# Kernel optimization log

Measured on AMD Instinct MI355X. Metric: run time of the kernel, lower is better.

Reference implementation:

```python
import jax, jax.numpy as jnp
import numpy as np

N_BINS = 64
SIGMA_SCALE = 0.5
EPS = 1e-8


def _radial_weights(H, W, dtype=jnp.float32):
    r_max = min(H, W) / 2.0 - 1.0
    yy, xx = jnp.meshgrid(jnp.arange(H, dtype=dtype), jnp.arange(W, dtype=dtype), indexing='ij')
    cx, cy = (W - 1) / 2.0, (H - 1) / 2.0
    r = jnp.sqrt((xx - cx) ** 2 + (yy - cy) ** 2)  # (H, W)
    edges = jnp.linspace(0.0, r_max, N_BINS + 1, dtype=dtype)
    centers = 0.5 * (edges[:-1] + edges[1:])  # (B,)
    bin_width = r_max / N_BINS
    sigma = SIGMA_SCALE * bin_width + EPS
    Wmat = jnp.exp(-0.5 * ((r[:, :, None] - centers) / sigma) ** 2)  # (H, W, B)
    return Wmat, centers


def setup_inputs() -> dict:
    key = jax.random.key(0)
    k1, k2 = jax.random.split(key)
    shape = (32, 12, 256, 256)
    pred = jax.random.uniform(k1, shape, dtype=jnp.float32)
    target = jax.random.uniform(k2, shape, dtype=jnp.float32)
    return {"pred": pred, "target": target}


def reference(pred, target):
    N, WVL, H, W = pred.shape
    Wmat, centers = _radial_weights(H, W, pred.dtype)
    Wflat = Wmat.reshape(H * W, N_BINS)            # (HW, B)
    den = jnp.maximum(Wflat.sum(axis=0), EPS)      # (B,)
    # broadcast-multiply-reduce expressed as a GEMM: (N*WVL, HW) @ (HW, B)
    Xf = pred.reshape(N, WVL, H * W)
    Yf = target.reshape(N, WVL, H * W)
    prof_pred = jnp.einsum('nwp,pb->nwb', Xf, Wflat) / den
    prof_targ = jnp.einsum('nwp,pb->nwb', Yf, Wflat) / den
    # bin_weight == 'r': weight by bin-center radius, normalized to unit mean
    w = centers[None, None, :]
    w = w / jnp.maximum(w.mean(axis=-1, keepdims=True), EPS)  # (1,1,B)
    # loss == 'fvu'
    y = prof_targ
    ybar = y.mean(axis=-1, keepdims=True)
    sse = (w * (prof_pred - y) ** 2).sum(axis=-1)
    ssy = jnp.maximum((w * (y - ybar) ** 2).sum(axis=-1), EPS)
    return (sse / ssy).mean()
```

## Files before the change

### kernel.cpp

```cpp
#include <hip/hip_runtime.h>
#include <math.h>


#define NBINS 64
#define WIN   8
#define G     4
#define NIMG  384
#define HDIM  256
#define WDIM  256
#define BANDS 8
#define BANDROWS 32

#define DEN_BANDS 128
#define DEN_ROWS  2

#define LOG2E 1.4426950408889634f
#define EXP_M4 0.018315638888734179f

__device__ __forceinline__ float fexp2(float x) {
#if __has_builtin(__builtin_amdgcn_exp2f)
  return __builtin_amdgcn_exp2f(x);
#else
  return exp2f(x);
#endif
}

__global__ __launch_bounds__(256) void radial_prof_kernel(
    const float* __restrict__ pred,
    const float* __restrict__ targ,
    float* __restrict__ prof)
{
  const int x     = threadIdx.x;
  const int band  = blockIdx.x & (BANDS - 1);
  const int chunk = blockIdx.x >> 3;
  const int g0    = chunk * G;

  __shared__ float hist[G][2][NBINS];
  for (int i = threadIdx.x; i < G * 2 * NBINS; i += 256) ((float*)hist)[i] = 0.f;
  __syncthreads();

  const float dx     = (float)x - 127.5f;
  const float dx2    = dx * dx;
  const int   y0     = band * BANDROWS;
  const float inv_bw = 64.0f / 127.0f;

  float acc[G][2][WIN];
  #pragma unroll
  for (int g = 0; g < G; ++g)
    #pragma unroll
    for (int i = 0; i < 2; ++i)
      #pragma unroll
      for (int s = 0; s < WIN; ++s) acc[g][i][s] = 0.f;

  int k0;
  {
    const float dy = (float)y0 - 127.5f;
    k0 = (int)floorf(sqrtf(dx2 + dy * dy) * inv_bw) - 3;
  }

  const size_t istr = (size_t)HDIM * WDIM;
  const float* pp = pred + (size_t)g0 * istr + (size_t)y0 * WDIM + x;
  const float* tp = targ + (size_t)g0 * istr + (size_t)y0 * WDIM + x;

  for (int yi = 0; yi < BANDROWS; ++yi) {
    const float dy = (float)(y0 + yi) - 127.5f;
    const float r  = sqrtf(dx2 + dy * dy);
    const float u  = r * inv_bw;
    const float fl = floorf(u);
    const int   k  = (int)fl - 3;

    if (k != k0) {
      if (k == k0 + 1) {
        if ((unsigned)k0 < NBINS) {
          #pragma unroll
          for (int g = 0; g < G; ++g) {
            atomicAdd(&hist[g][0][k0], acc[g][0][0]);
            atomicAdd(&hist[g][1][k0], acc[g][1][0]);
          }
        }
        #pragma unroll
        for (int g = 0; g < G; ++g)
          #pragma unroll
          for (int i = 0; i < 2; ++i) {
            #pragma unroll
            for (int s = 0; s < WIN - 1; ++s) acc[g][i][s] = acc[g][i][s + 1];
            acc[g][i][WIN - 1] = 0.f;
          }
      } else if (k == k0 - 1) {
        const int bh = k0 + WIN - 1;
        if ((unsigned)bh < NBINS) {
          #pragma unroll
          for (int g = 0; g < G; ++g) {
            atomicAdd(&hist[g][0][bh], acc[g][0][WIN - 1]);
            atomicAdd(&hist[g][1][bh], acc[g][1][WIN - 1]);
          }
        }
        #pragma unroll
        for (int g = 0; g < G; ++g)
          #pragma unroll
          for (int i = 0; i < 2; ++i) {
            #pragma unroll
            for (int s = WIN - 1; s > 0; --s) acc[g][i][s] = acc[g][i][s - 1];
            acc[g][i][0] = 0.f;
          }
      } else {
        #pragma unroll
        for (int s = 0; s < WIN; ++s) {
          const int b = k0 + s;
          if ((unsigned)b < NBINS) {
            #pragma unroll
            for (int g = 0; g < G; ++g) {
              atomicAdd(&hist[g][0][b], acc[g][0][s]);
              atomicAdd(&hist[g][1][b], acc[g][1][s]);
            }
          }
        }
        #pragma unroll
        for (int g = 0; g < G; ++g)
          #pragma unroll
          for (int i = 0; i < 2; ++i)
            #pragma unroll
            for (int s = 0; s < WIN; ++s) acc[g][i][s] = 0.f;
      }
      k0 = k;
    }

    if (k0 < NBINS) {
      const float t0 = (u - fl) + 2.5f;
      float w = fexp2(-(2.0f * LOG2E) * t0 * t0);
      float m = fexp2((4.0f * t0 - 2.0f) * LOG2E);
      float xp[G], xt[G];
      #pragma unroll
      for (int g = 0; g < G; ++g) {
        xp[g] = pp[(size_t)g * istr];
        xt[g] = tp[(size_t)g * istr];
      }
      #pragma unroll
      for (int s = 0; s < WIN; ++s) {
        #pragma unroll
        for (int g = 0; g < G; ++g) {
          acc[g][0][s] = fmaf(w, xp[g], acc[g][0][s]);
          acc[g][1][s] = fmaf(w, xt[g], acc[g][1][s]);
        }
        w *= m;
        m *= EXP_M4;
      }
    }
    pp += WDIM; tp += WDIM;
  }

  #pragma unroll
  for (int s = 0; s < WIN; ++s) {
    const int b = k0 + s;
    if ((unsigned)b < NBINS) {
      #pragma unroll
      for (int g = 0; g < G; ++g) {
        atomicAdd(&hist[g][0][b], acc[g][0][s]);
        atomicAdd(&hist[g][1][b], acc[g][1][s]);
      }
    }
  }
  __syncthreads();

  for (int i = threadIdx.x; i < G * 2 * NBINS; i += 256)
    atomicAdd(&prof[(size_t)g0 * 2 * NBINS + i], ((float*)hist)[i]);
}

__global__ __launch_bounds__(256) void den_kernel(float* __restrict__ den)
{
  const int x    = threadIdx.x;
  const int band = blockIdx.x;
  __shared__ float hist[NBINS];
  if (threadIdx.x < NBINS) hist[threadIdx.x] = 0.f;
  __syncthreads();

  const float dx     = (float)x - 127.5f;
  const float dx2    = dx * dx;
  const int   y0     = band * DEN_ROWS;
  const float inv_bw = 64.0f / 127.0f;

  float acc[WIN];
  #pragma unroll
  for (int s = 0; s < WIN; ++s) acc[s] = 0.f;

  int k0;
  {
    const float dy = (float)y0 - 127.5f;
    k0 = (int)floorf(sqrtf(dx2 + dy * dy) * inv_bw) - 3;
  }

  for (int yi = 0; yi < DEN_ROWS; ++yi) {
    const float dy = (float)(y0 + yi) - 127.5f;
    const float r  = sqrtf(dx2 + dy * dy);
    const float u  = r * inv_bw;
    const float fl = floorf(u);
    const int   k  = (int)fl - 3;

    if (k != k0) {
      if (k == k0 + 1) {
        if ((unsigned)k0 < NBINS) atomicAdd(&hist[k0], acc[0]);
        #pragma unroll
        for (int s = 0; s < WIN - 1; ++s) acc[s] = acc[s + 1];
        acc[WIN - 1] = 0.f;
      } else if (k == k0 - 1) {
        const int bh = k0 + WIN - 1;
        if ((unsigned)bh < NBINS) atomicAdd(&hist[bh], acc[WIN - 1]);
        #pragma unroll
        for (int s = WIN - 1; s > 0; --s) acc[s] = acc[s - 1];
        acc[0] = 0.f;
      } else {
        #pragma unroll
        for (int s = 0; s < WIN; ++s) {
          const int b = k0 + s;
          if ((unsigned)b < NBINS) atomicAdd(&hist[b], acc[s]);
          acc[s] = 0.f;
        }
      }
      k0 = k;
    }

    if (k0 < NBINS) {
      const float t0 = (u - fl) + 2.5f;
      float w = fexp2(-(2.0f * LOG2E) * t0 * t0);
      float m = fexp2((4.0f * t0 - 2.0f) * LOG2E);
      #pragma unroll
      for (int s = 0; s < WIN; ++s) {
        acc[s] += w;
        w *= m;
        m *= EXP_M4;
      }
    }
  }

  #pragma unroll
  for (int s = 0; s < WIN; ++s) {
    const int b = k0 + s;
    if ((unsigned)b < NBINS) atomicAdd(&hist[b], acc[s]);
  }
  __syncthreads();
  if (threadIdx.x < NBINS) atomicAdd(&den[threadIdx.x], hist[threadIdx.x]);
}

__global__ __launch_bounds__(NIMG) void loss_kernel(
    const float* __restrict__ prof,
    const float* __restrict__ den,
    float* __restrict__ out)
{
  __shared__ float dsh[NBINS];
  __shared__ float red[NIMG];
  const int tid = threadIdx.x;
  if (tid < NBINS) dsh[tid] = 1.0f / fmaxf(den[tid], 1e-8f);
  __syncthreads();

  const float bw = 127.0f / 64.0f;
  const float* base = prof + (size_t)tid * (2 * NBINS);

  float tsum = 0.f;
  for (int b = 0; b < NBINS; ++b) tsum += base[NBINS + b] * dsh[b];
  const float ybar = tsum * (1.0f / NBINS);

  float sse = 0.f, ssy = 0.f;
  for (int b = 0; b < NBINS; ++b) {
    const float wb = ((float)b + 0.5f) * bw * (1.0f / 63.5f);
    const float P  = base[b] * dsh[b];
    const float T  = base[NBINS + b] * dsh[b];
    const float d1 = P - T;
    const float d2 = T - ybar;
    sse = fmaf(wb * d1, d1, sse);
    ssy = fmaf(wb * d2, d2, ssy);
  }
  red[tid] = sse / fmaxf(ssy, 1e-8f);
  __syncthreads();

  for (int s = 256; s > 0; s >>= 1) {
    if (tid < s && tid + s < NIMG) red[tid] += red[tid + s];
    __syncthreads();
  }
  if (tid == 0) out[0] = red[0] * (1.0f / NIMG);
}

extern "C" void kernel_launch(void* const* d_in, const int* in_sizes, int n_in,
                              void* d_out, int out_size, void* d_ws, size_t ws_size,
                              hipStream_t stream) {
  const float* pred = (const float*)d_in[0];
  const float* targ = (const float*)d_in[1];

  float* prof = (float*)d_ws;
  float* den  = prof + (size_t)NIMG * 2 * NBINS;

  hipMemsetAsync(d_ws, 0, ((size_t)NIMG * 2 * NBINS + NBINS) * sizeof(float), stream);

  den_kernel<<<DEN_BANDS, 256, 0, stream>>>(den);
  radial_prof_kernel<<<(NIMG / G) * BANDS, 256, 0, stream>>>(pred, targ, prof);
  loss_kernel<<<1, NIMG, 0, stream>>>(prof, den, (float*)d_out);
}
```

Before: 317.4 us.

## Split profile kernel into more bands and software-prefetch next row loads

Raises the band count from 8 to 32 (8 rows each), giving four times as many blocks, and sets a min-blocks-per-SM hint on launch bounds. The row loop is fully unrolled and double-buffers the pred/target loads, fetching row y+1 while row y is accumulated. The squared radius is now updated incrementally instead of recomputed each row. More bands means more shared-histogram flushes and more global atomics per image, and the occupancy hint may force register spills given the 64-float accumulator array.

```diff
diff --git a/kernel.cpp b/kernel.cpp
--- a/kernel.cpp
+++ b/kernel.cpp
@@ -8,8 +8,8 @@
 #define NIMG  384
 #define HDIM  256
 #define WDIM  256
-#define BANDS 8
-#define BANDROWS 32
+#define BANDS 32
+#define BANDROWS 8
 
 #define DEN_BANDS 128
 #define DEN_ROWS  2
@@ -25,14 +25,14 @@
 #endif
 }
 
-__global__ __launch_bounds__(256) void radial_prof_kernel(
+__global__ __launch_bounds__(256, 4) void radial_prof_kernel(
     const float* __restrict__ pred,
     const float* __restrict__ targ,
     float* __restrict__ prof)
 {
   const int x     = threadIdx.x;
   const int band  = blockIdx.x & (BANDS - 1);
-  const int chunk = blockIdx.x >> 3;
+  const int chunk = blockIdx.x >> 5;
   const int g0    = chunk * G;
 
   __shared__ float hist[G][2][NBINS];
@@ -52,22 +52,36 @@
       #pragma unroll
       for (int s = 0; s < WIN; ++s) acc[g][i][s] = 0.f;
 
-  int k0;
-  {
-    const float dy = (float)y0 - 127.5f;
-    k0 = (int)floorf(sqrtf(dx2 + dy * dy) * inv_bw) - 3;
-  }
+  float dy  = (float)y0 - 127.5f;
+  float rsq = dx2 + dy * dy;
+  int k0 = (int)floorf(sqrtf(rsq) * inv_bw) - 3;
 
   const size_t istr = (size_t)HDIM * WDIM;
   const float* pp = pred + (size_t)g0 * istr + (size_t)y0 * WDIM + x;
   const float* tp = targ + (size_t)g0 * istr + (size_t)y0 * WDIM + x;
 
+  float cp[G], ct[G], np[G], nt[G];
+  #pragma unroll
+  for (int g = 0; g < G; ++g) {
+    cp[g] = pp[(size_t)g * istr];
+    ct[g] = tp[(size_t)g * istr];
+  }
+
+  #pragma unroll
   for (int yi = 0; yi < BANDROWS; ++yi) {
-    const float dy = (float)(y0 + yi) - 127.5f;
-    const float r  = sqrtf(dx2 + dy * dy);
-    const float u  = r * inv_bw;
+    if (yi + 1 < BANDROWS) {
+      #pragma unroll
+      for (int g = 0; g < G; ++g) {
+        np[g] = pp[WDIM + (size_t)g * istr];
+        nt[g] = tp[WDIM + (size_t)g * istr];
+      }
+    }
+
+    const float u  = sqrtf(rsq) * inv_bw;
     const float fl = floorf(u);
     const int   k  = (int)fl - 3;
+    rsq += 2.0f * dy + 1.0f;
+    dy  += 1.0f;
 
     if (k != k0) {
       if (k == k0 + 1) {
@@ -129,24 +143,21 @@
       const float t0 = (u - fl) + 2.5f;
       float w = fexp2(-(2.0f * LOG2E) * t0 * t0);
       float m = fexp2((4.0f * t0 - 2.0f) * LOG2E);
-      float xp[G], xt[G];
-      #pragma unroll
-      for (int g = 0; g < G; ++g) {
-        xp[g] = pp[(size_t)g * istr];
-        xt[g] = tp[(size_t)g * istr];
-      }
       #pragma unroll
       for (int s = 0; s < WIN; ++s) {
         #pragma unroll
         for (int g = 0; g < G; ++g) {
-          acc[g][0][s] = fmaf(w, xp[g], acc[g][0][s]);
-          acc[g][1][s] = fmaf(w, xt[g], acc[g][1][s]);
+          acc[g][0][s] = fmaf(w, cp[g], acc[g][0][s]);
+          acc[g][1][s] = fmaf(w, ct[g], acc[g][1][s]);
         }
         w *= m;
         m *= EXP_M4;
       }
     }
+
     pp += WDIM; tp += WDIM;
+    #pragma unroll
+    for (int g = 0; g < G; ++g) { cp[g] = np[g]; ct[g] = nt[g]; }
   }
 
   #pragma unroll
```

New measurement: 541.8 us. 1.71x slower.
